# Optimization experiments

Hardware: AMD Instinct MI355X
Metric: run time of the kernel (lower is better)

The kernel has to match this reference:

```python
import jax, jax.numpy as jnp
import numpy as np

HEADS = 4
EPS = 1e-5

def _layernorm(x, g, b):
    mu = jnp.mean(x, axis=-1, keepdims=True)
    var = jnp.var(x, axis=-1, keepdims=True)
    return (x - mu) / jnp.sqrt(var + EPS) * g + b

def setup_inputs() -> dict:
    key = jax.random.key(0)
    ks = jax.random.split(key, 16)
    N, dim, k, G = 400000, 256, 1, 4096
    h = jax.random.normal(ks[0], (N, dim), dtype=jnp.float32)
    batch = jnp.sort(jax.random.randint(ks[1], (N,), 0, G).astype(jnp.int64))
    s = 1.0 / np.sqrt(dim)
    return {
        "h": h,
        "batch": batch,
        "num_graphs": G,
        "seed": jax.random.normal(ks[2], (k, dim), dtype=jnp.float32),
        "in_proj_w": jax.random.uniform(ks[3], (3 * dim, dim), minval=-s, maxval=s, dtype=jnp.float32),
        "in_proj_b": jnp.zeros((3 * dim,), jnp.float32),
        "out_w": jax.random.uniform(ks[4], (dim, dim), minval=-s, maxval=s, dtype=jnp.float32),
        "out_b": jnp.zeros((dim,), jnp.float32),
        "w1": jax.random.uniform(ks[5], (4 * dim, dim), minval=-s, maxval=s, dtype=jnp.float32),
        "b1": jnp.zeros((4 * dim,), jnp.float32),
        "w2": jax.random.uniform(ks[6], (dim, 4 * dim), minval=-1.0 / np.sqrt(4 * dim), maxval=1.0 / np.sqrt(4 * dim), dtype=jnp.float32),
        "b2": jnp.zeros((dim,), jnp.float32),
        "g1": jnp.ones((dim,), jnp.float32),
        "beta1": jnp.zeros((dim,), jnp.float32),
        "g2": jnp.ones((dim,), jnp.float32),
        "beta2": jnp.zeros((dim,), jnp.float32),
    }

def reference(h, batch, num_graphs, seed, in_proj_w, in_proj_b, out_w, out_b,
              w1, b1, w2, b2, g1, beta1, g2, beta2):
    N, dim = h.shape
    k = seed.shape[0]
    hd = dim // HEADS
    G = num_graphs
    # q/k/v projections (torch MHA packed in_proj: rows [0:dim]=Q, [dim:2dim]=K, [2dim:]=V)
    q = seed @ in_proj_w[:dim].T + in_proj_b[:dim]                 # [k, dim]
    kk = h @ in_proj_w[dim:2 * dim].T + in_proj_b[dim:2 * dim]     # [N, dim]
    vv = h @ in_proj_w[2 * dim:].T + in_proj_b[2 * dim:]           # [N, dim]
    qh = q.reshape(k, HEADS, hd).transpose(1, 0, 2)                # [H, k, hd]
    kh = kk.reshape(N, HEADS, hd)                                  # [N, H, hd]
    vh = vv.reshape(N, HEADS, hd)                                  # [N, H, hd]
    scale = 1.0 / np.sqrt(hd)
    scores = jnp.einsum('hkd,nhd->nhk', qh, kh) * scale            # [N, H, k]
    # segment softmax over nodes of each graph
    smax = jax.ops.segment_max(scores, batch, num_segments=G)      # [G, H, k]
    e = jnp.exp(scores - smax[batch])                              # [N, H, k]
    denom = jax.ops.segment_sum(e, batch, num_segments=G)          # [G, H, k]
    wv = jax.ops.segment_sum(e[:, :, :, None] * vh[:, :, None, :], batch, num_segments=G)  # [G, H, k, hd]
    attn = jnp.where(denom[..., None] > 0, wv / jnp.maximum(denom, 1e-9)[..., None], 0.0)
    attn = attn.transpose(0, 2, 1, 3).reshape(G, k, dim)           # [G, k, dim]
    o = attn @ out_w.T + out_b                                     # [G, k, dim]
    x = _layernorm(o + seed[None, :, :], g1, beta1)
    f = jax.nn.relu(x @ w1.T + b1) @ w2.T + b2
    x = _layernorm(x + f, g2, beta2)
    # empty graphs output zeros (matches torch loop)
    count = jax.ops.segment_sum(jnp.ones((N,), jnp.float32), batch, num_segments=G)
    return jnp.where((count > 0)[:, None, None], x, 0.0)
```

## Files before the change

### kernel.cpp

```cpp
#include <hip/hip_runtime.h>
#include <hip/hip_bf16.h>


#define DIM 256
#define CHUNK 32

typedef short bf16x8 __attribute__((ext_vector_type(8)));
typedef float f32x4  __attribute__((ext_vector_type(4)));
#define MFMA16(a, b, c) __builtin_amdgcn_mfma_f32_16x16x32_bf16(a, b, c, 0, 0, 0)

#define OFF_C      0
#define OFF_D      1024
#define OFF_CONST  1040
#define OFF_P2B    2048
#define OFF_W1B    133120
#define OFF_W2B    264192
#define OFF_TB     395264
#define OFF_CNT    6162432

__global__ __launch_bounds__(256) void prep_all_kernel(
    const float* __restrict__ seed, const float* __restrict__ ipw,
    const float* __restrict__ ipb, const float* __restrict__ out_w,
    const float* __restrict__ out_b, const float* __restrict__ w1,
    const float* __restrict__ w2,
    float* __restrict__ cvec, float* __restrict__ dconst,
    float* __restrict__ constvec, __hip_bfloat16* __restrict__ P2b,
    __hip_bfloat16* __restrict__ w1b, __hip_bfloat16* __restrict__ w2b)
{
    int b = blockIdx.x, t = threadIdx.x;
    __shared__ float q_s[DIM];
    if (b < 1024) {
        int i = b >> 2, hD = b & 3;
        float a = 0.f;
        for (int j = 0; j < 64; ++j)
            a += out_w[i * DIM + hD * 64 + j]
               * ipw[(size_t)(2 * DIM + hD * 64 + j) * DIM + t];
        P2b[(size_t)i * 1024 + hD * DIM + t] = __float2bfloat16(a);
    } else if (b == 1024) {
        const float scale = 0.125f;
        float acc = ipb[t];
        for (int d = 0; d < DIM; ++d) acc += seed[d] * ipw[t * DIM + d];
        q_s[t] = acc;
        __syncthreads();
        for (int hh = 0; hh < 4; ++hh) {
            float a = 0.f;
            for (int j = 0; j < 64; ++j)
                a += q_s[hh * 64 + j] * ipw[(size_t)(DIM + hh * 64 + j) * DIM + t];
            cvec[hh * DIM + t] = a * scale;
        }
        if (t < 4) {
            float a = 0.f;
            for (int j = 0; j < 64; ++j)
                a += q_s[t * 64 + j] * ipb[DIM + t * 64 + j];
            dconst[t] = a * scale;
        }
        float cc = out_b[t];
        for (int c = 0; c < DIM; ++c)
            cc += out_w[t * DIM + c] * ipb[2 * DIM + c];
        constvec[t] = cc;
    } else if (b < 1153) {
        int base = (b - 1025) * 2048 + t;
        for (int i = 0; i < 8; ++i)
            w1b[base + i * 256] = __float2bfloat16(w1[base + i * 256]);
    } else {
        int base = (b - 1153) * 2048 + t;
        for (int i = 0; i < 8; ++i)
            w2b[base + i * 256] = __float2bfloat16(w2[base + i * 256]);
    }
}

__global__ __launch_bounds__(256) void attn_pool_kernel(
    const float* __restrict__ hmat, const int* __restrict__ batch,
    const float* __restrict__ cvec, const float* __restrict__ dconst,
    __hip_bfloat16* __restrict__ Tb, int* __restrict__ cnt, int N)
{
    int g = blockIdx.x;
    int tid = threadIdx.x;
    int lane = tid & 63, wave = tid >> 6;

    __shared__ float hbuf[CHUNK][DIM];
    __shared__ float4 esc[CHUNK];
    __shared__ float lred[4][4];

    int s, e;
    { int l = 0, r = N;
      while (l < r) { int m = (l + r) >> 1; if (batch[m] < g) l = m + 1; else r = m; }
      s = l; }
    { int l = s, r = N;
      while (l < r) { int m = (l + r) >> 1; if (batch[m] < g + 1) l = m + 1; else r = m; }
      e = l; }

    if (tid == 0) cnt[g] = e - s;
    size_t tbase = (size_t)g * 1024;
    if (e == s) {
        __hip_bfloat16 z = __float2bfloat16(0.f);
        Tb[tbase + tid] = z; Tb[tbase + 256 + tid] = z;
        Tb[tbase + 512 + tid] = z; Tb[tbase + 768 + tid] = z;
        return;
    }

    int hh = lane & 3, seg = lane >> 2;
    const float* cb = cvec + hh * DIM + seg * 16;
    float4 cr0 = *(const float4*)(cb + 0);
    float4 cr1 = *(const float4*)(cb + 4);
    float4 cr2 = *(const float4*)(cb + 8);
    float4 cr3 = *(const float4*)(cb + 12);
    float dc_mine = dconst[hh];

    float S0 = 0.f, S1 = 0.f, S2 = 0.f, S3 = 0.f;
    float lp = 0.f;

    float4 rbuf[8];
    {
        int cc0 = min(CHUNK, e - s);
#pragma unroll
        for (int i = 0; i < 8; ++i) {
            int idx = tid + i * 256;
            if (idx < cc0 * 64) {
                int j = idx >> 6, q4 = idx & 63;
                rbuf[i] = *(const float4*)&hmat[(size_t)(s + j) * DIM + q4 * 4];
            }
        }
    }

    for (int n0 = s; n0 < e; n0 += CHUNK) {
        int ccnt = min(CHUNK, e - n0);
#pragma unroll
        for (int i = 0; i < 8; ++i) {
            int idx = tid + i * 256;
            if (idx < ccnt * 64) {
                int j = idx >> 6, q4 = idx & 63;
                *(float4*)&hbuf[j][q4 * 4] = rbuf[i];
            }
        }
        __syncthreads();

        int n1 = n0 + CHUNK;
        if (n1 < e) {
            int cn = min(CHUNK, e - n1);
#pragma unroll
            for (int i = 0; i < 8; ++i) {
                int idx = tid + i * 256;
                if (idx < cn * 64) {
                    int j = idx >> 6, q4 = idx & 63;
                    rbuf[i] = *(const float4*)&hmat[(size_t)(n1 + j) * DIM + q4 * 4];
                }
            }
        }

        for (int j = wave; j < ccnt; j += 4) {
            const float* hb = &hbuf[j][seg * 16];
            float4 h0 = *(const float4*)(hb + 0);
            float4 h1 = *(const float4*)(hb + 4);
            float4 h2 = *(const float4*)(hb + 8);
            float4 h3 = *(const float4*)(hb + 12);
            float p = h0.x * cr0.x + h0.y * cr0.y + h0.z * cr0.z + h0.w * cr0.w
                    + h1.x * cr1.x + h1.y * cr1.y + h1.z * cr1.z + h1.w * cr1.w
                    + h2.x * cr2.x + h2.y * cr2.y + h2.z * cr2.z + h2.w * cr2.w
                    + h3.x * cr3.x + h3.y * cr3.y + h3.z * cr3.z + h3.w * cr3.w;
            p += __shfl_xor(p, 4);
            p += __shfl_xor(p, 8);
            p += __shfl_xor(p, 16);
            p += __shfl_xor(p, 32);
            if (lane < 4) {
                float ev = __expf(p + dc_mine);
                ((float*)&esc[j])[lane] = ev;
                lp += ev;
            }
        }
        __syncthreads();

        for (int j = 0; j < ccnt; ++j) {
            float4 e4 = esc[j];
            float hv = hbuf[j][tid];
            S0 = fmaf(e4.x, hv, S0); S1 = fmaf(e4.y, hv, S1);
            S2 = fmaf(e4.z, hv, S2); S3 = fmaf(e4.w, hv, S3);
        }
        __syncthreads();
    }

    if (lane < 4) lred[wave][lane] = lp;
    __syncthreads();
    float l0 = lred[0][0] + lred[1][0] + lred[2][0] + lred[3][0];
    float l1 = lred[0][1] + lred[1][1] + lred[2][1] + lred[3][1];
    float l2 = lred[0][2] + lred[1][2] + lred[2][2] + lred[3][2];
    float l3 = lred[0][3] + lred[1][3] + lred[2][3] + lred[3][3];
    Tb[tbase + tid]       = __float2bfloat16(S0 / l0);
    Tb[tbase + 256 + tid] = __float2bfloat16(S1 / l1);
    Tb[tbase + 512 + tid] = __float2bfloat16(S2 / l2);
    Tb[tbase + 768 + tid] = __float2bfloat16(S3 / l3);
}

__global__ __launch_bounds__(256) void mlp_fused_kernel(
    const __hip_bfloat16* __restrict__ Tb, const __hip_bfloat16* __restrict__ P2b,
    const float* __restrict__ constvec, const float* __restrict__ seed,
    const float* __restrict__ g1, const float* __restrict__ be1,
    const __hip_bfloat16* __restrict__ w1b, const float* __restrict__ b1,
    const __hip_bfloat16* __restrict__ w2b, const float* __restrict__ b2,
    const float* __restrict__ g2, const float* __restrict__ be2,
    const int* __restrict__ cnt, float* __restrict__ outp)
{
    int m0 = blockIdx.x * 16;
    int tid = threadIdx.x;
    int w = tid >> 6, lane = tid & 63, quad = lane >> 4, l16 = lane & 15;

    __shared__ float x1s[16][260];
    __shared__ __hip_bfloat16 x1bs[16][264];
    __shared__ __hip_bfloat16 us[16][1032];
    __shared__ float redS[4][16], redQ[4][16];

    f32x4 acc0[4];
#pragma unroll
    for (int i = 0; i < 4; ++i) acc0[i] = (f32x4){0.f, 0.f, 0.f, 0.f};
    const __hip_bfloat16* Ap0 = Tb + (size_t)(m0 + l16) * 1024 + quad * 8;
    const __hip_bfloat16* Bp0 = P2b + (size_t)(w * 64 + l16) * 1024 + quad * 8;
    for (int k0 = 0; k0 < 1024; k0 += 32) {
        bf16x8 a = *(const bf16x8*)(Ap0 + k0);
#pragma unroll
        for (int nt = 0; nt < 4; ++nt) {
            bf16x8 b = *(const bf16x8*)(Bp0 + (size_t)nt * 16 * 1024 + k0);
            acc0[nt] = MFMA16(a, b, acc0[nt]);
        }
    }
    float v0[4][4];
    {
        float sum[4] = {0, 0, 0, 0}, sq[4] = {0, 0, 0, 0};
#pragma unroll
        for (int nt = 0; nt < 4; ++nt) {
            int col = w * 64 + nt * 16 + l16;
            float cv = constvec[col] + seed[col];
#pragma unroll
            for (int r = 0; r < 4; ++r) {
                float x = acc0[nt][r] + cv;
                v0[nt][r] = x; sum[r] += x; sq[r] += x * x;
            }
        }
#pragma unroll
        for (int r = 0; r < 4; ++r) {
            float s_ = sum[r], q_ = sq[r];
            s_ += __shfl_xor(s_, 1);  q_ += __shfl_xor(q_, 1);
            s_ += __shfl_xor(s_, 2);  q_ += __shfl_xor(q_, 2);
            s_ += __shfl_xor(s_, 4);  q_ += __shfl_xor(q_, 4);
            s_ += __shfl_xor(s_, 8);  q_ += __shfl_xor(q_, 8);
            if (l16 == 0) { redS[w][quad * 4 + r] = s_; redQ[w][quad * 4 + r] = q_; }
        }
    }
    __syncthreads();
    {
        float mu_r[4], rs_r[4];
#pragma unroll
        for (int r = 0; r < 4; ++r) {
            int row = quad * 4 + r;
            float s_ = redS[0][row] + redS[1][row] + redS[2][row] + redS[3][row];
            float q_ = redQ[0][row] + redQ[1][row] + redQ[2][row] + redQ[3][row];
            float mu = s_ * (1.f / 256);
            float var = q_ * (1.f / 256) - mu * mu;
            mu_r[r] = mu;
            rs_r[r] = rsqrtf(fmaxf(var, 0.f) + 1e-5f);
        }
#pragma unroll
        for (int nt = 0; nt < 4; ++nt) {
            int col = w * 64 + nt * 16 + l16;
            float gg = g1[col], bb = be1[col];
#pragma unroll
            for (int r = 0; r < 4; ++r) {
                int row = quad * 4 + r;
                float y = (v0[nt][r] - mu_r[r]) * rs_r[r] * gg + bb;
                x1s[row][col] = y;
                x1bs[row][col] = __float2bfloat16(y);
            }
        }
    }
    __syncthreads();

    f32x4 acc1[16];
#pragma unroll
    for (int i = 0; i < 16; ++i) acc1[i] = (f32x4){0.f, 0.f, 0.f, 0.f};
    const __hip_bfloat16* Bp1 = w1b + (size_t)(w * 256 + l16) * 256 + quad * 8;
#pragma unroll
    for (int k0 = 0; k0 < 256; k0 += 32) {
        bf16x8 a = *(const bf16x8*)&x1bs[l16][quad * 8 + k0];
#pragma unroll
        for (int nt = 0; nt < 16; ++nt) {
            bf16x8 b = *(const bf16x8*)(Bp1 + (size_t)nt * 16 * 256 + k0);
            acc1[nt] = MFMA16(a, b, acc1[nt]);
        }
    }
#pragma unroll
    for (int nt = 0; nt < 16; ++nt) {
        int col = w * 256 + nt * 16 + l16;
        float bb = b1[col];
#pragma unroll
        for (int r = 0; r < 4; ++r) {
            int row = quad * 4 + r;
            us[row][col] = __float2bfloat16(fmaxf(acc1[nt][r] + bb, 0.f));
        }
    }
    __syncthreads();

    f32x4 acc2[4];
#pragma unroll
    for (int i = 0; i < 4; ++i) acc2[i] = (f32x4){0.f, 0.f, 0.f, 0.f};
    const __hip_bfloat16* Bp2 = w2b + (size_t)(w * 64 + l16) * 1024 + quad * 8;
    for (int k0 = 0; k0 < 1024; k0 += 32) {
        bf16x8 a = *(const bf16x8*)&us[l16][quad * 8 + k0];
#pragma unroll
        for (int nt = 0; nt < 4; ++nt) {
            bf16x8 b = *(const bf16x8*)(Bp2 + (size_t)nt * 16 * 1024 + k0);
            acc2[nt] = MFMA16(a, b, acc2[nt]);
        }
    }
    float v2[4][4];
    {
        float sum[4] = {0, 0, 0, 0}, sq[4] = {0, 0, 0, 0};
#pragma unroll
        for (int nt = 0; nt < 4; ++nt) {
            int col = w * 64 + nt * 16 + l16;
            float bb = b2[col];
#pragma unroll
            for (int r = 0; r < 4; ++r) {
                int row = quad * 4 + r;
                float x = acc2[nt][r] + bb + x1s[row][col];
                v2[nt][r] = x; sum[r] += x; sq[r] += x * x;
            }
        }
#pragma unroll
        for (int r = 0; r < 4; ++r) {
            float s_ = sum[r], q_ = sq[r];
            s_ += __shfl_xor(s_, 1);  q_ += __shfl_xor(q_, 1);
            s_ += __shfl_xor(s_, 2);  q_ += __shfl_xor(q_, 2);
            s_ += __shfl_xor(s_, 4);  q_ += __shfl_xor(q_, 4);
            s_ += __shfl_xor(s_, 8);  q_ += __shfl_xor(q_, 8);
            if (l16 == 0) { redS[w][quad * 4 + r] = s_; redQ[w][quad * 4 + r] = q_; }
        }
    }
    __syncthreads();
    {
#pragma unroll
        for (int r = 0; r < 4; ++r) {
            int row = quad * 4 + r;
            float s_ = redS[0][row] + redS[1][row] + redS[2][row] + redS[3][row];
            float q_ = redQ[0][row] + redQ[1][row] + redQ[2][row] + redQ[3][row];
            float mu = s_ * (1.f / 256);
            float var = q_ * (1.f / 256) - mu * mu;
            float rs = rsqrtf(fmaxf(var, 0.f) + 1e-5f);
            int gr = m0 + row;
            float mask = (cnt[gr] > 0) ? 1.f : 0.f;
#pragma unroll
            for (int nt = 0; nt < 4; ++nt) {
                int col = w * 64 + nt * 16 + l16;
                float y = ((v2[nt][r] - mu) * rs * g2[col] + be2[col]) * mask;
                outp[(size_t)gr * 256 + col] = y;
            }
        }
    }
}

extern "C" void kernel_launch(void* const* d_in, const int* in_sizes, int n_in,
                              void* d_out, int out_size, void* d_ws, size_t ws_size,
                              hipStream_t stream) {
    const float* h     = (const float*)d_in[0];
    const int*   batch = (const int*)d_in[1];
    const float* seed  = (const float*)d_in[3];
    const float* ipw   = (const float*)d_in[4];
    const float* ipb   = (const float*)d_in[5];
    const float* out_w = (const float*)d_in[6];
    const float* out_b = (const float*)d_in[7];
    const float* w1    = (const float*)d_in[8];
    const float* b1    = (const float*)d_in[9];
    const float* w2    = (const float*)d_in[10];
    const float* b2    = (const float*)d_in[11];
    const float* g1    = (const float*)d_in[12];
    const float* be1   = (const float*)d_in[13];
    const float* g2    = (const float*)d_in[14];
    const float* be2   = (const float*)d_in[15];

    int N = in_sizes[1];
    int G = out_size / DIM;

    float* ws = (float*)d_ws;
    float* cvec     = ws + OFF_C;
    float* dconst   = ws + OFF_D;
    float* constvec = ws + OFF_CONST;
    __hip_bfloat16* P2b = (__hip_bfloat16*)(ws + OFF_P2B);
    __hip_bfloat16* w1b = (__hip_bfloat16*)(ws + OFF_W1B);
    __hip_bfloat16* w2b = (__hip_bfloat16*)(ws + OFF_W2B);
    __hip_bfloat16* Tb  = (__hip_bfloat16*)(ws + OFF_TB);
    int*   cnt      = (int*)(ws + OFF_CNT);

    prep_all_kernel<<<1281, 256, 0, stream>>>(seed, ipw, ipb, out_w, out_b, w1, w2,
                                              cvec, dconst, constvec, P2b, w1b, w2b);
    attn_pool_kernel<<<G, 256, 0, stream>>>(h, batch, cvec, dconst, Tb, cnt, N);
    mlp_fused_kernel<<<G / 16, 256, 0, stream>>>(Tb, P2b, constvec, seed, g1, be1,
                                                 w1b, b1, w2b, b2, g2, be2, cnt,
                                                 (float*)d_out);
}
```

Before: 808.9 us.

## Precompute graph start offsets and stream node rows directly into double-buffered LDS

Graph segment boundaries are now computed once, in extra blocks of the prep kernel, by scanning the sorted batch array. This replaces the two per-block binary searches over the batch array in the attention kernel. The attention kernel also drops register-staged prefetching and loads each chunk of h rows straight into LDS with global_load_lds, using two LDS buffers so the next chunk arrives while the current one is processed. That removes one barrier per chunk, but doubling the LDS footprint can lower occupancy, and correctness depends on the compiler waiting for the async LDS loads before the barrier.

```diff
diff --git a/kernel.cpp b/kernel.cpp
--- a/kernel.cpp
+++ b/kernel.cpp
@@ -8,6 +8,11 @@
 typedef short bf16x8 __attribute__((ext_vector_type(8)));
 typedef float f32x4  __attribute__((ext_vector_type(4)));
 #define MFMA16(a, b, c) __builtin_amdgcn_mfma_f32_16x16x32_bf16(a, b, c, 0, 0, 0)
+
+#define GLOAD_LDS16(gp, lp)                                          \
+    __builtin_amdgcn_global_load_lds(                                \
+        (const __attribute__((address_space(1))) void*)(gp),         \
+        (__attribute__((address_space(3))) void*)(lp), 16, 0, 0)
 
 #define OFF_C      0
 #define OFF_D      1024
@@ -17,15 +22,17 @@
 #define OFF_W2B    264192
 #define OFF_TB     395264
 #define OFF_CNT    6162432
+#define OFF_STARTS 6166528
 
 __global__ __launch_bounds__(256) void prep_all_kernel(
     const float* __restrict__ seed, const float* __restrict__ ipw,
     const float* __restrict__ ipb, const float* __restrict__ out_w,
     const float* __restrict__ out_b, const float* __restrict__ w1,
-    const float* __restrict__ w2,
+    const float* __restrict__ w2, const int* __restrict__ batch,
     float* __restrict__ cvec, float* __restrict__ dconst,
     float* __restrict__ constvec, __hip_bfloat16* __restrict__ P2b,
-    __hip_bfloat16* __restrict__ w1b, __hip_bfloat16* __restrict__ w2b)
+    __hip_bfloat16* __restrict__ w1b, __hip_bfloat16* __restrict__ w2b,
+    int* __restrict__ starts, int N, int G)
 {
     int b = blockIdx.x, t = threadIdx.x;
     __shared__ float q_s[DIM];
@@ -62,34 +69,36 @@
         int base = (b - 1025) * 2048 + t;
         for (int i = 0; i < 8; ++i)
             w1b[base + i * 256] = __float2bfloat16(w1[base + i * 256]);
-    } else {
+    } else if (b < 1281) {
         int base = (b - 1153) * 2048 + t;
         for (int i = 0; i < 8; ++i)
             w2b[base + i * 256] = __float2bfloat16(w2[base + i * 256]);
+    } else {
+        int n = (b - 1281) * 256 + t;
+        if (n < N) {
+            int bn = batch[n];
+            int bp = (n == 0) ? -1 : batch[n - 1];
+            for (int gg = bp + 1; gg <= bn; ++gg) starts[gg] = n;
+            if (n == N - 1)
+                for (int gg = bn + 1; gg <= G; ++gg) starts[gg] = N;
+        }
     }
 }
 
 __global__ __launch_bounds__(256) void attn_pool_kernel(
-    const float* __restrict__ hmat, const int* __restrict__ batch,
+    const float* __restrict__ hmat, const int* __restrict__ starts,
     const float* __restrict__ cvec, const float* __restrict__ dconst,
-    __hip_bfloat16* __restrict__ Tb, int* __restrict__ cnt, int N)
+    __hip_bfloat16* __restrict__ Tb, int* __restrict__ cnt)
 {
     int g = blockIdx.x;
     int tid = threadIdx.x;
     int lane = tid & 63, wave = tid >> 6;
 
-    __shared__ float hbuf[CHUNK][DIM];
+    __shared__ float hbuf[2][CHUNK][DIM];
     __shared__ float4 esc[CHUNK];
     __shared__ float lred[4][4];
 
-    int s, e;
-    { int l = 0, r = N;
-      while (l < r) { int m = (l + r) >> 1; if (batch[m] < g) l = m + 1; else r = m; }
-      s = l; }
-    { int l = s, r = N;
-      while (l < r) { int m = (l + r) >> 1; if (batch[m] < g + 1) l = m + 1; else r = m; }
-      e = l; }
-
+    int s = starts[g], e = starts[g + 1];
     if (tid == 0) cnt[g] = e - s;
     size_t tbase = (size_t)g * 1024;
     if (e == s) {
@@ -110,29 +119,20 @@
     float S0 = 0.f, S1 = 0.f, S2 = 0.f, S3 = 0.f;
     float lp = 0.f;
 
-    float4 rbuf[8];
-    {
-        int cc0 = min(CHUNK, e - s);
+    {
+        int c0 = min(CHUNK, e - s);
 #pragma unroll
         for (int i = 0; i < 8; ++i) {
-            int idx = tid + i * 256;
-            if (idx < cc0 * 64) {
-                int j = idx >> 6, q4 = idx & 63;
-                rbuf[i] = *(const float4*)&hmat[(size_t)(s + j) * DIM + q4 * 4];
-            }
-        }
-    }
-
-    for (int n0 = s; n0 < e; n0 += CHUNK) {
+            int r = wave * 8 + i;
+            if (r < c0)
+                GLOAD_LDS16(&hmat[(size_t)(s + r) * DIM + lane * 4],
+                            &hbuf[0][r][0]);
+        }
+    }
+
+    int cur = 0;
+    for (int n0 = s; n0 < e; n0 += CHUNK, cur ^= 1) {
         int ccnt = min(CHUNK, e - n0);
-#pragma unroll
-        for (int i = 0; i < 8; ++i) {
-            int idx = tid + i * 256;
-            if (idx < ccnt * 64) {
-                int j = idx >> 6, q4 = idx & 63;
-                *(float4*)&hbuf[j][q4 * 4] = rbuf[i];
-            }
-        }
         __syncthreads();
 
         int n1 = n0 + CHUNK;
@@ -140,16 +140,15 @@
             int cn = min(CHUNK, e - n1);
 #pragma unroll
             for (int i = 0; i < 8; ++i) {
-                int idx = tid + i * 256;
-                if (idx < cn * 64) {
-                    int j = idx >> 6, q4 = idx & 63;
-                    rbuf[i] = *(const float4*)&hmat[(size_t)(n1 + j) * DIM + q4 * 4];
-                }
+                int r = wave * 8 + i;
+                if (r < cn)
+                    GLOAD_LDS16(&hmat[(size_t)(n1 + r) * DIM + lane * 4],
+                                &hbuf[cur ^ 1][r][0]);
             }
         }
 
         for (int j = wave; j < ccnt; j += 4) {
-            const float* hb = &hbuf[j][seg * 16];
+            const float* hb = &hbuf[cur][j][seg * 16];
             float4 h0 = *(const float4*)(hb + 0);
             float4 h1 = *(const float4*)(hb + 4);
             float4 h2 = *(const float4*)(hb + 8);
@@ -172,13 +171,13 @@
 
         for (int j = 0; j < ccnt; ++j) {
             float4 e4 = esc[j];
-            float hv = hbuf[j][tid];
+            float hv = hbuf[cur][j][tid];
             S0 = fmaf(e4.x, hv, S0); S1 = fmaf(e4.y, hv, S1);
             S2 = fmaf(e4.z, hv, S2); S3 = fmaf(e4.w, hv, S3);
         }
-        __syncthreads();
-    }
-
+    }
+
+    __syncthreads();
     if (lane < 4) lred[wave][lane] = lp;
     __syncthreads();
     float l0 = lred[0][0] + lred[1][0] + lred[2][0] + lred[3][0];
@@ -387,10 +386,13 @@
     __hip_bfloat16* w2b = (__hip_bfloat16*)(ws + OFF_W2B);
     __hip_bfloat16* Tb  = (__hip_bfloat16*)(ws + OFF_TB);
     int*   cnt      = (int*)(ws + OFF_CNT);
-
-    prep_all_kernel<<<1281, 256, 0, stream>>>(seed, ipw, ipb, out_w, out_b, w1, w2,
-                                              cvec, dconst, constvec, P2b, w1b, w2b);
-    attn_pool_kernel<<<G, 256, 0, stream>>>(h, batch, cvec, dconst, Tb, cnt, N);
+    int*   startsp  = (int*)(ws + OFF_STARTS);
+
+    int sblocks = (N + 255) / 256;
+    prep_all_kernel<<<1281 + sblocks, 256, 0, stream>>>(
+        seed, ipw, ipb, out_w, out_b, w1, w2, batch,
+        cvec, dconst, constvec, P2b, w1b, w2b, startsp, N, G);
+    attn_pool_kernel<<<G, 256, 0, stream>>>(h, startsp, cvec, dconst, Tb, cnt);
     mlp_fused_kernel<<<G / 16, 256, 0, stream>>>(Tb, P2b, constvec, seed, g1, be1,
                                                  w1b, b1, w2b, b2, g2, be2, cnt,
                                                  (float*)d_out);
```

After: 675.1 us. -16.5%, faster.
